# Kernel tuning notes

Measured on AMD Instinct MI355X. Metric: run time of the kernel, lower is better.

Reference implementation:

```python
import jax, jax.numpy as jnp
import numpy as np
import math

B, T, C = 8, 4096, 768
N_LAYER, LAYER_ID = 12, 6
LN_EPS = 1e-5


def wkv(w, u, k, v):
    """Numerically-stable RWKV-4 WKV recurrence.
    w, u: [C] (per-channel decay / bonus); k, v: [B, T, C] -> y: [B, T, C]."""
    kT = jnp.swapaxes(k, 0, 1)  # [T, B, C]
    vT = jnp.swapaxes(v, 0, 1)

    def step(carry, kv):
        aa, bb, pp = carry
        kt, vt = kv
        ww = u + kt
        p = jnp.maximum(pp, ww)
        e1 = jnp.exp(pp - p)
        e2 = jnp.exp(ww - p)
        y = (e1 * aa + e2 * vt) / (e1 * bb + e2)
        ww2 = w + pp
        p2 = jnp.maximum(ww2, kt)
        e1b = jnp.exp(ww2 - p2)
        e2b = jnp.exp(kt - p2)
        return (e1b * aa + e2b * vt, e1b * bb + e2b, p2), y

    zeros = jnp.zeros((k.shape[0], k.shape[2]), k.dtype)
    init = (zeros, zeros, jnp.full_like(zeros, -1e38))
    _, yT = jax.lax.scan(step, init, (kT, vT))
    return jnp.swapaxes(yT, 0, 1)  # [B, T, C]


def setup_inputs():
    key = jax.random.key(0)
    ks = jax.random.split(key, 8)
    # fancy init of spatial_decay / spatial_first (matches torch __init__)
    ratio = LAYER_ID / max(N_LAYER - 1, 1)
    h = np.arange(C, dtype=np.float64)
    decay = -5 + 8 * (h / max(C - 1, 1)) ** (0.7 + 1.3 * ratio)
    zigzag = np.array([(i + 1) % 3 - 1 for i in range(C)], dtype=np.float64) * 0.5
    first = np.ones(C) * math.log(0.3) + zigzag
    s = C ** -0.5
    return {
        "x_seq": jax.random.normal(ks[0], (B, T, C), jnp.float32),
        "scan_indices": jax.random.permutation(ks[1], T).astype(jnp.int32),
        "spatial_decay": jnp.asarray(decay, jnp.float32),
        "spatial_first": jnp.asarray(first, jnp.float32),
        "Wk": jax.random.normal(ks[2], (C, C), jnp.float32) * s,
        "Wv": jax.random.normal(ks[3], (C, C), jnp.float32) * s,
        "Wr": jax.random.normal(ks[4], (C, C), jnp.float32) * s,
        "Wo": jax.random.normal(ks[5], (C, C), jnp.float32) * s,
        "ln_g": jnp.ones((C,), jnp.float32),
        "ln_b": jnp.zeros((C,), jnp.float32),
    }


def reference(x_seq, scan_indices, spatial_decay, spatial_first, Wk, Wv, Wr, Wo, ln_g, ln_b):
    L = x_seq.shape[1]
    k = jnp.einsum('blc,dc->bld', x_seq, Wk)
    v = jnp.einsum('blc,dc->bld', x_seq, Wv)
    r = jnp.einsum('blc,dc->bld', x_seq, Wr)
    sr = jax.nn.sigmoid(r)
    # gather along sequence per scan order
    k_s = jnp.take(k, scan_indices, axis=1)
    v_s = jnp.take(v, scan_indices, axis=1)
    rwkv = wkv(spatial_decay / L, spatial_first / L, k_s, v_s)
    inv = jnp.argsort(scan_indices)
    rwkv = jnp.take(rwkv, inv, axis=1)
    # LayerNorm (key_norm)
    mu = jnp.mean(rwkv, axis=-1, keepdims=True)
    var = jnp.var(rwkv, axis=-1, keepdims=True)
    rwkv = (rwkv - mu) * jax.lax.rsqrt(var + LN_EPS) * ln_g + ln_b
    rwkv = sr * rwkv
    return jnp.einsum('blc,dc->bld', rwkv, Wo)
```

## Files before the change

kernel.cpp:

```cpp
#include <hip/hip_runtime.h>
#include <cstddef>
#include <cstdint>

#define B_DIM 8
#define T_SEQ 4096
#define C_DIM 768
#define M_ROWS (B_DIM * T_SEQ)
#define CC (C_DIM * C_DIM)
#define NCH 32
#define CHL (T_SEQ / NCH)

using bf16x8 = __attribute__((ext_vector_type(8))) short;
using f32x4  = __attribute__((ext_vector_type(4))) float;

static __device__ __forceinline__ unsigned short f2bf(float f) {
  unsigned int u = __float_as_uint(f);
  return (unsigned short)((u + 0x7fffu + ((u >> 16) & 1u)) >> 16);
}
static __device__ __forceinline__ float bf2f(unsigned short s) {
  return __uint_as_float(((unsigned int)s) << 16);
}

static __device__ __forceinline__ void gload_lds16(const void* g, void* l) {
  __builtin_amdgcn_global_load_lds(
      (const __attribute__((address_space(1))) unsigned int*)g,
      (__attribute__((address_space(3))) unsigned int*)l, 16, 0, 0);
}

__global__ __launch_bounds__(256) void convert_x(
    const float4* __restrict__ x, ushort4* __restrict__ xh)
{
  int i = blockIdx.x * 256 + threadIdx.x;
  float4 v = x[i];
  ushort4 h;
  h.x = f2bf(v.x); h.y = f2bf(v.y); h.z = f2bf(v.z); h.w = f2bf(v.w);
  xh[i] = h;
}

__global__ __launch_bounds__(256) void convert_w4(
    const float4* __restrict__ w0, const float4* __restrict__ w1,
    const float4* __restrict__ w2, const float4* __restrict__ w3,
    ushort4* __restrict__ dst)
{
  const int z = blockIdx.y;
  const float4* __restrict__ src = (z == 0) ? w0 : (z == 1) ? w1 : (z == 2) ? w2 : w3;
  int i = blockIdx.x * 256 + threadIdx.x;
  float4 v = src[i];
  ushort4 h;
  h.x = f2bf(v.x); h.y = f2bf(v.y); h.z = f2bf(v.z); h.w = f2bf(v.w);
  dst[(size_t)z * (CC / 4) + i] = h;
}

#define STG_A(DB, TAU, KH) do {                                            \
    const int ko_ = (TAU) * 64 + (KH) * 32;                                \
    short* d_ = lds + (((DB) + (KH) * 16384 + wave * 1024) >> 1);          \
    gload_lds16(pA_h0 + ko_, d_);                                          \
    gload_lds16(pA_h1 + ko_, d_ + 4096);                                   \
  } while (0)
#define STG_B(DB, TAU, KH) do {                                            \
    const int ko_ = (TAU) * 64 + (KH) * 32;                                \
    short* d_ = lds + (((DB) + 32768 + (KH) * 16384 + wave * 1024) >> 1);  \
    gload_lds16(pW_h0 + ko_, d_);                                          \
    gload_lds16(pW_h1 + ko_, d_ + 4096);                                   \
  } while (0)

#define MPHASE(DB, KHOFF, STAGE, CKPT)                                     \
  {                                                                        \
    _Pragma("unroll")                                                      \
    for (int mi = 0; mi < 8; ++mi)                                         \
      a[mi] = *(const bf16x8*)(lds +                                       \
          (((DB) + (KHOFF) + aoff + mi * 1024) >> 1));                     \
    _Pragma("unroll")                                                      \
    for (int ni = 0; ni < 4; ++ni)                                         \
      b[ni] = *(const bf16x8*)(lds +                                       \
          (((DB) + 32768 + (KHOFF) + boff + ni * 1024) >> 1));             \
    STAGE;                                                                 \
    __builtin_amdgcn_s_barrier();                                          \
    asm volatile("s_waitcnt lgkmcnt(0)" ::: "memory");                     \
    __builtin_amdgcn_sched_barrier(0);                                     \
    __builtin_amdgcn_s_setprio(1);                                         \
    _Pragma("unroll")                                                      \
    for (int mi = 0; mi < 8; ++mi)                                         \
      _Pragma("unroll")                                                    \
      for (int ni = 0; ni < 4; ++ni)                                       \
        acc[mi][ni] = __builtin_amdgcn_mfma_f32_16x16x32_bf16(             \
            a[mi], b[ni], acc[mi][ni], 0, 0, 0);                           \
    __builtin_amdgcn_s_setprio(0);                                         \
    CKPT;                                                                  \
    __builtin_amdgcn_s_barrier();                                          \
  }

template<int MODE>
__global__ __launch_bounds__(512, 2) void gemm8p(
    const short* __restrict__ A, const short* __restrict__ Wb,
    unsigned short* __restrict__ OK, unsigned short* __restrict__ OV,
    unsigned short* __restrict__ OSR, float* __restrict__ Oout)
{
  extern __shared__ short lds[];
  const int K = C_DIM;
  constexpr int NWN = (MODE == 0) ? 9 : 3;
  constexpr int CPX = (MODE == 0) ? 144 : 48;

  int f  = blockIdx.x + blockIdx.y * NWN;
  int wg = (f & 7) * CPX + (f >> 3);
  const int n0 = (wg % NWN) * 256;
  const int m0 = (wg / NWN) * 256;

  const int tid  = threadIdx.x;
  const int lane = tid & 63, wave = tid >> 6;
  const int wr = wave >> 2, wc = wave & 3;
  const int lr = lane & 15, lk = lane >> 4;

  const int aswz = lk ^ ((lr >> 1) & 3);
  const int aoff = wr * 8192 + lr * 64 + aswz * 16;
  const int boff = (wc >> 1) * 8192 + (wc & 1) * 4096 + lr * 64 + aswz * 16;

  const int srow = wave * 16 + (lane >> 2);
  const int skq  = (lane & 3) ^ ((lane >> 3) & 3);
  const short* pA_h0 = A + (size_t)(m0 + srow) * K + skq * 8;
  const short* pA_h1 = pA_h0 + (size_t)128 * K;
  const short* pW_h0 = Wb + (size_t)(n0 + srow) * K + skq * 8;
  const short* pW_h1 = pW_h0 + (size_t)128 * K;

  f32x4 acc[8][4];
#pragma unroll
  for (int i = 0; i < 8; ++i)
#pragma unroll
    for (int j = 0; j < 4; ++j) acc[i][j] = (f32x4){0.f, 0.f, 0.f, 0.f};

  STG_A(0, 0, 0); STG_B(0, 0, 0); STG_A(0, 0, 1); STG_B(0, 0, 1);
  STG_A(65536, 1, 0); STG_B(65536, 1, 0); STG_A(65536, 1, 1); STG_B(65536, 1, 1);
  asm volatile("s_waitcnt vmcnt(8)" ::: "memory");
  __builtin_amdgcn_s_barrier();

  bf16x8 a[8], b[4];
#pragma unroll
  for (int it = 0; it < 6; ++it) {
    MPHASE(0, 0,
        if (it >= 1) { STG_A(65536, 2 * it + 1, 1); STG_B(65536, 2 * it + 1, 1); }, )
    MPHASE(0, 16384,
        if (it < 5) { STG_A(0, 2 * it + 2, 0); STG_B(0, 2 * it + 2, 0); },
        if (it < 5) { asm volatile("s_waitcnt vmcnt(4)" ::: "memory"); }
        else        { asm volatile("s_waitcnt vmcnt(0)" ::: "memory"); })
    MPHASE(65536, 0,
        if (it < 5) { STG_A(0, 2 * it + 2, 1); STG_B(0, 2 * it + 2, 1); }, )
    MPHASE(65536, 16384,
        if (it < 5) { STG_A(65536, 2 * it + 3, 0); STG_B(65536, 2 * it + 3, 0); },
        if (it < 5) { asm volatile("s_waitcnt vmcnt(4)" ::: "memory"); })
  }

  if (MODE == 0) {
    const int which = n0 / 768;
    const int nc = (n0 % 768) + wc * 64;
    unsigned short* __restrict__ D = (which == 0) ? OK : (which == 1) ? OV : OSR;
#pragma unroll
    for (int mi = 0; mi < 8; ++mi)
#pragma unroll
      for (int ni = 0; ni < 4; ++ni) {
        const int row = m0 + wr * 128 + mi * 16 + lk * 4;
        const int col = nc + ni * 16 + lr;
#pragma unroll
        for (int j = 0; j < 4; ++j) {
          float v = acc[mi][ni][j];
          if (which == 2) v = 1.f / (1.f + __expf(-v));
          D[(size_t)(row + j) * C_DIM + col] = f2bf(v);
        }
      }
  } else {
#pragma unroll
    for (int mi = 0; mi < 8; ++mi)
#pragma unroll
      for (int ni = 0; ni < 4; ++ni) {
        const int row = m0 + wr * 128 + mi * 16 + lk * 4;
        const int col = n0 + wc * 64 + ni * 16 + lr;
#pragma unroll
        for (int j = 0; j < 4; ++j)
          Oout[(size_t)(row + j) * C_DIM + col] = acc[mi][ni][j];
      }
  }
}

#define P1_LOAD(kk_, vv_, base_)                                  \
  _Pragma("unroll") for (int j = 0; j < 8; ++j) {                 \
    int r_ = si[(base_) + j];                                     \
    kk_[j] = Kb[(size_t)r_ * C_DIM];                              \
    vv_[j] = Vb[(size_t)r_ * C_DIM];                              \
  }
#define P1_COMP(kk_, vv_)                                         \
  _Pragma("unroll") for (int j = 0; j < 8; ++j) {                 \
    float kt = bf2f(kk_[j]), vt = bf2f(vv_[j]);                   \
    float ww2 = w + pp; float p2 = fmaxf(ww2, kt);                \
    float e1b = __expf(ww2 - p2), e2b = __expf(kt - p2);          \
    aa = e1b * aa + e2b * vt; bb = e1b * bb + e2b; pp = p2;       \
  }

__global__ __launch_bounds__(256) void wkv_pass1(
    const unsigned short* __restrict__ Kin, const unsigned short* __restrict__ Vin,
    const int* __restrict__ sidx, const float* __restrict__ decay,
    float* __restrict__ aL, float* __restrict__ bL, float* __restrict__ pL)
{
  __shared__ int si[CHL];
  const int tid = threadIdx.x;
  const int ch = blockIdx.x, b = blockIdx.z;
  const int c = blockIdx.y * 256 + tid;
  if (tid < CHL) si[tid] = sidx[ch * CHL + tid];
  __syncthreads();
  const float w = decay[c] * (1.0f / (float)T_SEQ);
  const unsigned short* Kb = Kin + (size_t)b * T_SEQ * C_DIM + c;
  const unsigned short* Vb = Vin + (size_t)b * T_SEQ * C_DIM + c;
  float aa = 0.f, bb = 0.f, pp = -1e38f;
  unsigned short kA[8], vA[8], kB[8], vB[8];
  P1_LOAD(kA, vA, 0)
  for (int t0 = 0; t0 < CHL; t0 += 16) {
    P1_LOAD(kB, vB, t0 + 8)
    P1_COMP(kA, vA)
    if (t0 + 16 < CHL) { P1_LOAD(kA, vA, t0 + 16) }
    P1_COMP(kB, vB)
  }
  const int idx = (b * C_DIM + c) * NCH + ch;
  aL[idx] = aa; bL[idx] = bb; pL[idx] = pp;
}

__global__ __launch_bounds__(256) void wkv_scan(
    const float* __restrict__ aL, const float* __restrict__ bL,
    const float* __restrict__ pL,
    float* __restrict__ aI, float* __restrict__ bI, float* __restrict__ pI,
    const float* __restrict__ decay)
{
  const int g = blockIdx.x * 256 + threadIdx.x;
  const int c = g % C_DIM;
  const float wL = decay[c] * ((float)CHL / (float)T_SEQ);
  float aa = 0.f, bb = 0.f, pp = -1e38f;
  const int base = g * NCH;
  for (int ch = 0; ch < NCH; ++ch) {
    aI[base + ch] = aa; bI[base + ch] = bb; pI[base + ch] = pp;
    float p1 = pp + wL;
    float p2 = pL[base + ch];
    float p  = fmaxf(p1, p2);
    float e1 = __expf(p1 - p), e2 = __expf(p2 - p);
    aa = e1 * aa + e2 * aL[base + ch];
    bb = e1 * bb + e2 * bL[base + ch];
    pp = p;
  }
}

#define P2_LOAD(rr_, kk_, vv_, base_)                             \
  _Pragma("unroll") for (int j = 0; j < 8; ++j) {                 \
    int r_ = si[(base_) + j];                                     \
    rr_[j] = r_;                                                  \
    kk_[j] = Kb[(size_t)r_ * C_DIM];                              \
    vv_[j] = Vb[(size_t)r_ * C_DIM];                              \
  }
#define P2_COMP(rr_, kk_, vv_)                                    \
  _Pragma("unroll") for (int j = 0; j < 8; ++j) {                 \
    float kt = bf2f(kk_[j]), vt = bf2f(vv_[j]);                   \
    float ww = u + kt; float p = fmaxf(pp, ww);                   \
    float e1 = __expf(pp - p), e2 = __expf(ww - p);               \
    float y = (e1 * aa + e2 * vt) / (e1 * bb + e2);               \
    Yb[(size_t)rr_[j] * C_DIM] = f2bf(y);                         \
    float ww2 = w + pp; float p2 = fmaxf(ww2, kt);                \
    float e1b = __expf(ww2 - p2), e2b = __expf(kt - p2);          \
    aa = e1b * aa + e2b * vt; bb = e1b * bb + e2b; pp = p2;       \
  }

__global__ __launch_bounds__(256) void wkv_pass2(
    const unsigned short* __restrict__ Kin, const unsigned short* __restrict__ Vin,
    const int* __restrict__ sidx,
    const float* __restrict__ decay, const float* __restrict__ first,
    const float* __restrict__ aI, const float* __restrict__ bI,
    const float* __restrict__ pI, unsigned short* __restrict__ Y)
{
  __shared__ int si[CHL];
  const int tid = threadIdx.x;
  const int ch = blockIdx.x, b = blockIdx.z;
  const int c = blockIdx.y * 256 + tid;
  if (tid < CHL) si[tid] = sidx[ch * CHL + tid];
  __syncthreads();
  const float w = decay[c] * (1.0f / (float)T_SEQ);
  const float u = first[c] * (1.0f / (float)T_SEQ);
  const unsigned short* Kb = Kin + (size_t)b * T_SEQ * C_DIM + c;
  const unsigned short* Vb = Vin + (size_t)b * T_SEQ * C_DIM + c;
  unsigned short* Yb = Y + (size_t)b * T_SEQ * C_DIM + c;
  const int idx = (b * C_DIM + c) * NCH + ch;
  float aa = aI[idx], bb = bI[idx], pp = pI[idx];
  int rA[8], rB[8]; unsigned short kA[8], vA[8], kB[8], vB[8];
  P2_LOAD(rA, kA, vA, 0)
  for (int t0 = 0; t0 < CHL; t0 += 16) {
    P2_LOAD(rB, kB, vB, t0 + 8)
    P2_COMP(rA, kA, vA)
    if (t0 + 16 < CHL) { P2_LOAD(rA, kA, vA, t0 + 16) }
    P2_COMP(rB, kB, vB)
  }
}

__global__ __launch_bounds__(256) void ln_gate(
    const unsigned short* __restrict__ Y, const unsigned short* __restrict__ SR,
    const float* __restrict__ gam, const float* __restrict__ bet,
    unsigned short* __restrict__ G)
{
  const size_t row = blockIdx.x;
  const unsigned short* x = Y + row * C_DIM;
  const unsigned short* sr = SR + row * C_DIM;
  unsigned short* go = G + row * C_DIM;
  const int tid = threadIdx.x;

  float vals[3];
  float s = 0.f, s2 = 0.f;
#pragma unroll
  for (int j = 0; j < 3; ++j) {
    float v = bf2f(x[tid + j * 256]);
    vals[j] = v;
    s += v; s2 += v * v;
  }
#pragma unroll
  for (int off = 32; off >= 1; off >>= 1) {
    s  += __shfl_xor(s, off, 64);
    s2 += __shfl_xor(s2, off, 64);
  }
  __shared__ float red[8];
  const int wid = tid >> 6;
  if ((tid & 63) == 0) { red[wid] = s; red[wid + 4] = s2; }
  __syncthreads();
  s  = red[0] + red[1] + red[2] + red[3];
  s2 = red[4] + red[5] + red[6] + red[7];

  const float mu   = s * (1.f / (float)C_DIM);
  const float var  = s2 * (1.f / (float)C_DIM) - mu * mu;
  const float rsig = rsqrtf(var + 1e-5f);

#pragma unroll
  for (int j = 0; j < 3; ++j) {
    const int cc = tid + j * 256;
    float yv = (vals[j] - mu) * rsig * gam[cc] + bet[cc];
    go[cc] = f2bf(yv * bf2f(sr[cc]));
  }
}

extern "C" void kernel_launch(void* const* d_in, const int* in_sizes, int n_in,
                              void* d_out, int out_size, void* d_ws, size_t ws_size,
                              hipStream_t stream) {
  const float* x     = (const float*)d_in[0];
  const int*   sidx  = (const int*)  d_in[1];
  const float* decay = (const float*)d_in[2];
  const float* first = (const float*)d_in[3];
  const float* Wk    = (const float*)d_in[4];
  const float* Wv    = (const float*)d_in[5];
  const float* Wr    = (const float*)d_in[6];
  const float* Wo    = (const float*)d_in[7];
  const float* ln_g  = (const float*)d_in[8];
  const float* ln_b  = (const float*)d_in[9];
  float* out = (float*)d_out;

  const size_t NE = (size_t)M_ROWS * C_DIM;
  short* Whs  = (short*)d_ws;
  short* x_hi = Whs + 4 * (size_t)CC;
  unsigned short* Ybuf = (unsigned short*)x_hi;
  unsigned short* Kbuf = (unsigned short*)(x_hi + NE);
  unsigned short* Gbuf = Kbuf;
  unsigned short* Vbuf = Kbuf + NE;
  unsigned short* SRb  = Vbuf + NE;
  float* aL = (float*)(SRb + NE);
  float* bL = aL + 196608;
  float* pL = bL + 196608;
  float* aI = pL + 196608;
  float* bI = aI + 196608;
  float* pI = bI + 196608;

  (void)hipFuncSetAttribute(reinterpret_cast<const void*>(&gemm8p<0>),
                            hipFuncAttributeMaxDynamicSharedMemorySize, 131072);
  (void)hipFuncSetAttribute(reinterpret_cast<const void*>(&gemm8p<1>),
                            hipFuncAttributeMaxDynamicSharedMemorySize, 131072);

  convert_x<<<24576, 256, 0, stream>>>((const float4*)x, (ushort4*)x_hi);
  convert_w4<<<dim3(576, 4), 256, 0, stream>>>(
      (const float4*)Wk, (const float4*)Wv, (const float4*)Wr, (const float4*)Wo,
      (ushort4*)Whs);

  gemm8p<0><<<dim3(9, 128), 512, 131072, stream>>>(
      x_hi, Whs, Kbuf, Vbuf, SRb, nullptr);

  wkv_pass1<<<dim3(NCH, 3, B_DIM), 256, 0, stream>>>(Kbuf, Vbuf, sidx, decay, aL, bL, pL);
  wkv_scan<<<24, 256, 0, stream>>>(aL, bL, pL, aI, bI, pI, decay);
  wkv_pass2<<<dim3(NCH, 3, B_DIM), 256, 0, stream>>>(Kbuf, Vbuf, sidx, decay, first,
                                                     aI, bI, pI, Ybuf);
  ln_gate<<<M_ROWS, 256, 0, stream>>>(Ybuf, SRb, ln_g, ln_b, Gbuf);
  gemm8p<1><<<dim3(3, 128), 512, 131072, stream>>>(
      (const short*)Gbuf, Whs + 3 * (size_t)CC, nullptr, nullptr, nullptr, out);
}
```

Baseline: 319.6 us.

## Fuse LayerNorm and gating into WKV pass2; register-prefetch LDS fragments in GEMM

The WKV second pass now runs one 768-thread block per (chunk, batch), so each block holds a full row of channels. It computes LayerNorm and the sigmoid gate inline at each timestep using wave shuffles plus a block-level reduction, and writes the gated output directly, which removes the separate ln_gate kernel and its Y buffer round trip. The cost is a __syncthreads per timestep inside the serial recurrence. Separately, the GEMM main loop is restructured with double-buffered register fragments: the next K-slice is read from LDS while MFMAs run on the current one, with three stages of global-to-LDS prefetch and one barrier per phase instead of two.

```diff
diff --git a/kernel.cpp b/kernel.cpp
--- a/kernel.cpp
+++ b/kernel.cpp
@@ -63,35 +63,31 @@
     gload_lds16(pW_h0 + ko_, d_);                                          \
     gload_lds16(pW_h1 + ko_, d_ + 4096);                                   \
   } while (0)
-
-#define MPHASE(DB, KHOFF, STAGE, CKPT)                                     \
-  {                                                                        \
+#define STG_R(R) do {                                                      \
+    STG_A((((R) >> 1) & 1) * 65536, (R) >> 1, (R) & 1);                    \
+    STG_B((((R) >> 1) & 1) * 65536, (R) >> 1, (R) & 1);                    \
+  } while (0)
+
+#define READF(AA, BB, R) do {                                              \
+    const int db_ = (((R) >> 1) & 1) * 65536 + ((R) & 1) * 16384;          \
     _Pragma("unroll")                                                      \
     for (int mi = 0; mi < 8; ++mi)                                         \
-      a[mi] = *(const bf16x8*)(lds +                                       \
-          (((DB) + (KHOFF) + aoff + mi * 1024) >> 1));                     \
+      AA[mi] = *(const bf16x8*)(lds + ((db_ + aoff + mi * 1024) >> 1));    \
     _Pragma("unroll")                                                      \
     for (int ni = 0; ni < 4; ++ni)                                         \
-      b[ni] = *(const bf16x8*)(lds +                                       \
-          (((DB) + 32768 + (KHOFF) + boff + ni * 1024) >> 1));             \
-    STAGE;                                                                 \
-    __builtin_amdgcn_s_barrier();                                          \
-    asm volatile("s_waitcnt lgkmcnt(0)" ::: "memory");                     \
-    __builtin_amdgcn_sched_barrier(0);                                     \
-    __builtin_amdgcn_s_setprio(1);                                         \
+      BB[ni] = *(const bf16x8*)(lds + ((db_ + 32768 + boff + ni * 1024) >> 1)); \
+  } while (0)
+
+#define MM(AA, BB)                                                         \
     _Pragma("unroll")                                                      \
     for (int mi = 0; mi < 8; ++mi)                                         \
       _Pragma("unroll")                                                    \
       for (int ni = 0; ni < 4; ++ni)                                       \
         acc[mi][ni] = __builtin_amdgcn_mfma_f32_16x16x32_bf16(             \
-            a[mi], b[ni], acc[mi][ni], 0, 0, 0);                           \
-    __builtin_amdgcn_s_setprio(0);                                         \
-    CKPT;                                                                  \
-    __builtin_amdgcn_s_barrier();                                          \
-  }
+            AA[mi], BB[ni], acc[mi][ni], 0, 0, 0);
 
 template<int MODE>
-__global__ __launch_bounds__(512, 2) void gemm8p(
+__global__ __launch_bounds__(512, 2) void gemmPF(
     const short* __restrict__ A, const short* __restrict__ Wb,
     unsigned short* __restrict__ OK, unsigned short* __restrict__ OV,
     unsigned short* __restrict__ OSR, float* __restrict__ Oout)
@@ -128,25 +124,29 @@
 #pragma unroll
     for (int j = 0; j < 4; ++j) acc[i][j] = (f32x4){0.f, 0.f, 0.f, 0.f};
 
-  STG_A(0, 0, 0); STG_B(0, 0, 0); STG_A(0, 0, 1); STG_B(0, 0, 1);
-  STG_A(65536, 1, 0); STG_B(65536, 1, 0); STG_A(65536, 1, 1); STG_B(65536, 1, 1);
-  asm volatile("s_waitcnt vmcnt(8)" ::: "memory");
+  bf16x8 aX[8], bX[4], aY[8], bY[4];
+
+  STG_R(0); STG_R(1); STG_R(2);
+  asm volatile("s_waitcnt vmcnt(4)" ::: "memory");
   __builtin_amdgcn_s_barrier();
-
-  bf16x8 a[8], b[4];
-#pragma unroll
-  for (int it = 0; it < 6; ++it) {
-    MPHASE(0, 0,
-        if (it >= 1) { STG_A(65536, 2 * it + 1, 1); STG_B(65536, 2 * it + 1, 1); }, )
-    MPHASE(0, 16384,
-        if (it < 5) { STG_A(0, 2 * it + 2, 0); STG_B(0, 2 * it + 2, 0); },
-        if (it < 5) { asm volatile("s_waitcnt vmcnt(4)" ::: "memory"); }
-        else        { asm volatile("s_waitcnt vmcnt(0)" ::: "memory"); })
-    MPHASE(65536, 0,
-        if (it < 5) { STG_A(0, 2 * it + 2, 1); STG_B(0, 2 * it + 2, 1); }, )
-    MPHASE(65536, 16384,
-        if (it < 5) { STG_A(65536, 2 * it + 3, 0); STG_B(65536, 2 * it + 3, 0); },
-        if (it < 5) { asm volatile("s_waitcnt vmcnt(4)" ::: "memory"); })
+  __builtin_amdgcn_sched_barrier(0);
+  READF(aX, bX, 0);
+  __builtin_amdgcn_sched_barrier(0);
+
+#pragma unroll
+  for (int p = 0; p < 24; ++p) {
+    if (p < 23) {
+      if (p & 1) { READF(aX, bX, p + 1); } else { READF(aY, bY, p + 1); }
+    }
+    if (p <= 20) STG_R(p + 3);
+    __builtin_amdgcn_sched_barrier(0);
+    __builtin_amdgcn_s_setprio(1);
+    if (p & 1) { MM(aY, bY) } else { MM(aX, bX) }
+    __builtin_amdgcn_s_setprio(0);
+    if (p <= 20)      { asm volatile("s_waitcnt vmcnt(4)" ::: "memory"); }
+    else if (p == 21) { asm volatile("s_waitcnt vmcnt(0)" ::: "memory"); }
+    __builtin_amdgcn_s_barrier();
+    __builtin_amdgcn_sched_barrier(0);
   }
 
   if (MODE == 0) {
@@ -244,95 +244,81 @@
   }
 }
 
-#define P2_LOAD(rr_, kk_, vv_, base_)                             \
+#define P2F_LOAD(rr_, kk_, vv_, ss_, base_)                       \
   _Pragma("unroll") for (int j = 0; j < 8; ++j) {                 \
     int r_ = si[(base_) + j];                                     \
     rr_[j] = r_;                                                  \
     kk_[j] = Kb[(size_t)r_ * C_DIM];                              \
     vv_[j] = Vb[(size_t)r_ * C_DIM];                              \
-  }
-#define P2_COMP(rr_, kk_, vv_)                                    \
+    ss_[j] = Sb[(size_t)r_ * C_DIM];                              \
+  }
+
+#define P2F_COMP(rr_, kk_, vv_, ss_)                              \
   _Pragma("unroll") for (int j = 0; j < 8; ++j) {                 \
     float kt = bf2f(kk_[j]), vt = bf2f(vv_[j]);                   \
     float ww = u + kt; float p = fmaxf(pp, ww);                   \
     float e1 = __expf(pp - p), e2 = __expf(ww - p);               \
-    float y = (e1 * aa + e2 * vt) / (e1 * bb + e2);               \
-    Yb[(size_t)rr_[j] * C_DIM] = f2bf(y);                         \
+    float y = (e1 * aa + e2 * vt) / (e1 * bbs + e2);              \
+    float s1 = y, s2v = y * y;                                    \
+    _Pragma("unroll")                                             \
+    for (int off = 32; off >= 1; off >>= 1) {                     \
+      s1  += __shfl_xor(s1, off, 64);                             \
+      s2v += __shfl_xor(s2v, off, 64);                            \
+    }                                                             \
+    if (lane == 0) { red[j & 1][0][wid] = s1; red[j & 1][1][wid] = s2v; } \
+    __syncthreads();                                              \
+    float ts = 0.f, ts2 = 0.f;                                    \
+    _Pragma("unroll")                                             \
+    for (int wv = 0; wv < 12; ++wv) {                             \
+      ts  += red[j & 1][0][wv];                                   \
+      ts2 += red[j & 1][1][wv];                                   \
+    }                                                             \
+    const float mu  = ts * (1.f / (float)C_DIM);                  \
+    const float var = ts2 * (1.f / (float)C_DIM) - mu * mu;       \
+    const float rs  = rsqrtf(var + 1e-5f);                        \
+    const float yln = (y - mu) * rs * gg + bb0;                   \
+    Gb[(size_t)rr_[j] * C_DIM] = f2bf(yln * bf2f(ss_[j]));        \
     float ww2 = w + pp; float p2 = fmaxf(ww2, kt);                \
     float e1b = __expf(ww2 - p2), e2b = __expf(kt - p2);          \
-    aa = e1b * aa + e2b * vt; bb = e1b * bb + e2b; pp = p2;       \
-  }
-
-__global__ __launch_bounds__(256) void wkv_pass2(
+    aa = e1b * aa + e2b * vt; bbs = e1b * bbs + e2b; pp = p2;     \
+  }
+
+__global__ __launch_bounds__(768) void wkv_pass2_ln(
     const unsigned short* __restrict__ Kin, const unsigned short* __restrict__ Vin,
     const int* __restrict__ sidx,
     const float* __restrict__ decay, const float* __restrict__ first,
     const float* __restrict__ aI, const float* __restrict__ bI,
-    const float* __restrict__ pI, unsigned short* __restrict__ Y)
+    const float* __restrict__ pI,
+    const unsigned short* __restrict__ SR,
+    const float* __restrict__ gam, const float* __restrict__ bet,
+    unsigned short* __restrict__ G)
 {
   __shared__ int si[CHL];
+  __shared__ float red[2][2][12];
   const int tid = threadIdx.x;
-  const int ch = blockIdx.x, b = blockIdx.z;
-  const int c = blockIdx.y * 256 + tid;
+  const int ch = blockIdx.x, b = blockIdx.y;
   if (tid < CHL) si[tid] = sidx[ch * CHL + tid];
   __syncthreads();
+  const int c = tid;
+  const int lane = tid & 63, wid = tid >> 6;
   const float w = decay[c] * (1.0f / (float)T_SEQ);
   const float u = first[c] * (1.0f / (float)T_SEQ);
+  const float gg = gam[c], bb0 = bet[c];
   const unsigned short* Kb = Kin + (size_t)b * T_SEQ * C_DIM + c;
   const unsigned short* Vb = Vin + (size_t)b * T_SEQ * C_DIM + c;
-  unsigned short* Yb = Y + (size_t)b * T_SEQ * C_DIM + c;
+  const unsigned short* Sb = SR + (size_t)b * T_SEQ * C_DIM + c;
+  unsigned short* Gb = G + (size_t)b * T_SEQ * C_DIM + c;
   const int idx = (b * C_DIM + c) * NCH + ch;
-  float aa = aI[idx], bb = bI[idx], pp = pI[idx];
-  int rA[8], rB[8]; unsigned short kA[8], vA[8], kB[8], vB[8];
-  P2_LOAD(rA, kA, vA, 0)
+  float aa = aI[idx], bbs = bI[idx], pp = pI[idx];
+
+  int rA[8], rB[8];
+  unsigned short kA[8], vA[8], sA[8], kB[8], vB[8], sB[8];
+  P2F_LOAD(rA, kA, vA, sA, 0)
   for (int t0 = 0; t0 < CHL; t0 += 16) {
-    P2_LOAD(rB, kB, vB, t0 + 8)
-    P2_COMP(rA, kA, vA)
-    if (t0 + 16 < CHL) { P2_LOAD(rA, kA, vA, t0 + 16) }
-    P2_COMP(rB, kB, vB)
-  }
-}
-
-__global__ __launch_bounds__(256) void ln_gate(
-    const unsigned short* __restrict__ Y, const unsigned short* __restrict__ SR,
-    const float* __restrict__ gam, const float* __restrict__ bet,
-    unsigned short* __restrict__ G)
-{
-  const size_t row = blockIdx.x;
-  const unsigned short* x = Y + row * C_DIM;
-  const unsigned short* sr = SR + row * C_DIM;
-  unsigned short* go = G + row * C_DIM;
-  const int tid = threadIdx.x;
-
-  float vals[3];
-  float s = 0.f, s2 = 0.f;
-#pragma unroll
-  for (int j = 0; j < 3; ++j) {
-    float v = bf2f(x[tid + j * 256]);
-    vals[j] = v;
-    s += v; s2 += v * v;
-  }
-#pragma unroll
-  for (int off = 32; off >= 1; off >>= 1) {
-    s  += __shfl_xor(s, off, 64);
-    s2 += __shfl_xor(s2, off, 64);
-  }
-  __shared__ float red[8];
-  const int wid = tid >> 6;
-  if ((tid & 63) == 0) { red[wid] = s; red[wid + 4] = s2; }
-  __syncthreads();
-  s  = red[0] + red[1] + red[2] + red[3];
-  s2 = red[4] + red[5] + red[6] + red[7];
-
-  const float mu   = s * (1.f / (float)C_DIM);
-  const float var  = s2 * (1.f / (float)C_DIM) - mu * mu;
-  const float rsig = rsqrtf(var + 1e-5f);
-
-#pragma unroll
-  for (int j = 0; j < 3; ++j) {
-    const int cc = tid + j * 256;
-    float yv = (vals[j] - mu) * rsig * gam[cc] + bet[cc];
-    go[cc] = f2bf(yv * bf2f(sr[cc]));
+    P2F_LOAD(rB, kB, vB, sB, t0 + 8)
+    P2F_COMP(rA, kA, vA, sA)
+    if (t0 + 16 < CHL) { P2F_LOAD(rA, kA, vA, sA, t0 + 16) }
+    P2F_COMP(rB, kB, vB, sB)
   }
 }
 
@@ -354,21 +340,20 @@
   const size_t NE = (size_t)M_ROWS * C_DIM;
   short* Whs  = (short*)d_ws;
   short* x_hi = Whs + 4 * (size_t)CC;
-  unsigned short* Ybuf = (unsigned short*)x_hi;
   unsigned short* Kbuf = (unsigned short*)(x_hi + NE);
-  unsigned short* Gbuf = Kbuf;
   unsigned short* Vbuf = Kbuf + NE;
   unsigned short* SRb  = Vbuf + NE;
-  float* aL = (float*)(SRb + NE);
+  unsigned short* Gbuf = SRb + NE;
+  float* aL = (float*)(Gbuf + NE);
   float* bL = aL + 196608;
   float* pL = bL + 196608;
   float* aI = pL + 196608;
   float* bI = aI + 196608;
   float* pI = bI + 196608;
 
-  (void)hipFuncSetAttribute(reinterpret_cast<const void*>(&gemm8p<0>),
+  (void)hipFuncSetAttribute(reinterpret_cast<const void*>(&gemmPF<0>),
                             hipFuncAttributeMaxDynamicSharedMemorySize, 131072);
-  (void)hipFuncSetAttribute(reinterpret_cast<const void*>(&gemm8p<1>),
+  (void)hipFuncSetAttribute(reinterpret_cast<const void*>(&gemmPF<1>),
                             hipFuncAttributeMaxDynamicSharedMemorySize, 131072);
 
   convert_x<<<24576, 256, 0, stream>>>((const float4*)x, (ushort4*)x_hi);
@@ -376,14 +361,14 @@
       (const float4*)Wk, (const float4*)Wv, (const float4*)Wr, (const float4*)Wo,
       (ushort4*)Whs);
 
-  gemm8p<0><<<dim3(9, 128), 512, 131072, stream>>>(
+  gemmPF<0><<<dim3(9, 128), 512, 131072, stream>>>(
       x_hi, Whs, Kbuf, Vbuf, SRb, nullptr);
 
   wkv_pass1<<<dim3(NCH, 3, B_DIM), 256, 0, stream>>>(Kbuf, Vbuf, sidx, decay, aL, bL, pL);
   wkv_scan<<<24, 256, 0, stream>>>(aL, bL, pL, aI, bI, pI, decay);
-  wkv_pass2<<<dim3(NCH, 3, B_DIM), 256, 0, stream>>>(Kbuf, Vbuf, sidx, decay, first,
-                                                     aI, bI, pI, Ybuf);
-  ln_gate<<<M_ROWS, 256, 0, stream>>>(Ybuf, SRb, ln_g, ln_b, Gbuf);
-  gemm8p<1><<<dim3(3, 128), 512, 131072, stream>>>(
+  wkv_pass2_ln<<<dim3(NCH, B_DIM), 768, 0, stream>>>(
+      Kbuf, Vbuf, sidx, decay, first, aI, bI, pI, SRb, ln_g, ln_b, Gbuf);
+
+  gemmPF<1><<<dim3(3, 128), 512, 131072, stream>>>(
       (const short*)Gbuf, Whs + 3 * (size_t)CC, nullptr, nullptr, nullptr, out);
 }
```

Result: slower. 380.2 us (+18.9%).

## Double-buffer LDS fragment reads in registers and deepen the global prefetch

Applied to the files above, without the earlier changes.

Restructures the GEMM main loop into 24 half-tile phases. The LDS-to-register fragment reads for the next phase go into a second register set (aX/bX vs aY/bY), so they overlap the current MFMA block instead of waiting on lgkmcnt before the math. Global-to-LDS staging now runs three half-stages ahead, and there is one barrier per phase instead of two. The extra fragment registers raise register pressure at 2 blocks per CU, and the tighter buffer reuse distance could race if the wait counts are off.

```diff
diff --git a/kernel.cpp b/kernel.cpp
--- a/kernel.cpp
+++ b/kernel.cpp
@@ -63,35 +63,31 @@
     gload_lds16(pW_h0 + ko_, d_);                                          \
     gload_lds16(pW_h1 + ko_, d_ + 4096);                                   \
   } while (0)
-
-#define MPHASE(DB, KHOFF, STAGE, CKPT)                                     \
-  {                                                                        \
+#define STG_R(R) do {                                                      \
+    STG_A((((R) >> 1) & 1) * 65536, (R) >> 1, (R) & 1);                    \
+    STG_B((((R) >> 1) & 1) * 65536, (R) >> 1, (R) & 1);                    \
+  } while (0)
+
+#define READF(AA, BB, R) do {                                              \
+    const int db_ = (((R) >> 1) & 1) * 65536 + ((R) & 1) * 16384;          \
     _Pragma("unroll")                                                      \
     for (int mi = 0; mi < 8; ++mi)                                         \
-      a[mi] = *(const bf16x8*)(lds +                                       \
-          (((DB) + (KHOFF) + aoff + mi * 1024) >> 1));                     \
+      AA[mi] = *(const bf16x8*)(lds + ((db_ + aoff + mi * 1024) >> 1));    \
     _Pragma("unroll")                                                      \
     for (int ni = 0; ni < 4; ++ni)                                         \
-      b[ni] = *(const bf16x8*)(lds +                                       \
-          (((DB) + 32768 + (KHOFF) + boff + ni * 1024) >> 1));             \
-    STAGE;                                                                 \
-    __builtin_amdgcn_s_barrier();                                          \
-    asm volatile("s_waitcnt lgkmcnt(0)" ::: "memory");                     \
-    __builtin_amdgcn_sched_barrier(0);                                     \
-    __builtin_amdgcn_s_setprio(1);                                         \
+      BB[ni] = *(const bf16x8*)(lds + ((db_ + 32768 + boff + ni * 1024) >> 1)); \
+  } while (0)
+
+#define MM(AA, BB)                                                         \
     _Pragma("unroll")                                                      \
     for (int mi = 0; mi < 8; ++mi)                                         \
       _Pragma("unroll")                                                    \
       for (int ni = 0; ni < 4; ++ni)                                       \
         acc[mi][ni] = __builtin_amdgcn_mfma_f32_16x16x32_bf16(             \
-            a[mi], b[ni], acc[mi][ni], 0, 0, 0);                           \
-    __builtin_amdgcn_s_setprio(0);                                         \
-    CKPT;                                                                  \
-    __builtin_amdgcn_s_barrier();                                          \
-  }
+            AA[mi], BB[ni], acc[mi][ni], 0, 0, 0);
 
 template<int MODE>
-__global__ __launch_bounds__(512, 2) void gemm8p(
+__global__ __launch_bounds__(512, 2) void gemmPF(
     const short* __restrict__ A, const short* __restrict__ Wb,
     unsigned short* __restrict__ OK, unsigned short* __restrict__ OV,
     unsigned short* __restrict__ OSR, float* __restrict__ Oout)
@@ -128,25 +124,29 @@
 #pragma unroll
     for (int j = 0; j < 4; ++j) acc[i][j] = (f32x4){0.f, 0.f, 0.f, 0.f};
 
-  STG_A(0, 0, 0); STG_B(0, 0, 0); STG_A(0, 0, 1); STG_B(0, 0, 1);
-  STG_A(65536, 1, 0); STG_B(65536, 1, 0); STG_A(65536, 1, 1); STG_B(65536, 1, 1);
-  asm volatile("s_waitcnt vmcnt(8)" ::: "memory");
+  bf16x8 aX[8], bX[4], aY[8], bY[4];
+
+  STG_R(0); STG_R(1); STG_R(2);
+  asm volatile("s_waitcnt vmcnt(4)" ::: "memory");
   __builtin_amdgcn_s_barrier();
-
-  bf16x8 a[8], b[4];
-#pragma unroll
-  for (int it = 0; it < 6; ++it) {
-    MPHASE(0, 0,
-        if (it >= 1) { STG_A(65536, 2 * it + 1, 1); STG_B(65536, 2 * it + 1, 1); }, )
-    MPHASE(0, 16384,
-        if (it < 5) { STG_A(0, 2 * it + 2, 0); STG_B(0, 2 * it + 2, 0); },
-        if (it < 5) { asm volatile("s_waitcnt vmcnt(4)" ::: "memory"); }
-        else        { asm volatile("s_waitcnt vmcnt(0)" ::: "memory"); })
-    MPHASE(65536, 0,
-        if (it < 5) { STG_A(0, 2 * it + 2, 1); STG_B(0, 2 * it + 2, 1); }, )
-    MPHASE(65536, 16384,
-        if (it < 5) { STG_A(65536, 2 * it + 3, 0); STG_B(65536, 2 * it + 3, 0); },
-        if (it < 5) { asm volatile("s_waitcnt vmcnt(4)" ::: "memory"); })
+  __builtin_amdgcn_sched_barrier(0);
+  READF(aX, bX, 0);
+  __builtin_amdgcn_sched_barrier(0);
+
+#pragma unroll
+  for (int p = 0; p < 24; ++p) {
+    if (p < 23) {
+      if (p & 1) { READF(aX, bX, p + 1); } else { READF(aY, bY, p + 1); }
+    }
+    if (p <= 20) STG_R(p + 3);
+    __builtin_amdgcn_sched_barrier(0);
+    __builtin_amdgcn_s_setprio(1);
+    if (p & 1) { MM(aY, bY) } else { MM(aX, bX) }
+    __builtin_amdgcn_s_setprio(0);
+    if (p <= 20)      { asm volatile("s_waitcnt vmcnt(4)" ::: "memory"); }
+    else if (p == 21) { asm volatile("s_waitcnt vmcnt(0)" ::: "memory"); }
+    __builtin_amdgcn_s_barrier();
+    __builtin_amdgcn_sched_barrier(0);
   }
 
   if (MODE == 0) {
@@ -366,9 +366,9 @@
   float* bI = aI + 196608;
   float* pI = bI + 196608;
 
-  (void)hipFuncSetAttribute(reinterpret_cast<const void*>(&gemm8p<0>),
+  (void)hipFuncSetAttribute(reinterpret_cast<const void*>(&gemmPF<0>),
                             hipFuncAttributeMaxDynamicSharedMemorySize, 131072);
-  (void)hipFuncSetAttribute(reinterpret_cast<const void*>(&gemm8p<1>),
+  (void)hipFuncSetAttribute(reinterpret_cast<const void*>(&gemmPF<1>),
                             hipFuncAttributeMaxDynamicSharedMemorySize, 131072);
 
   convert_x<<<24576, 256, 0, stream>>>((const float4*)x, (ushort4*)x_hi);
@@ -376,7 +376,7 @@
       (const float4*)Wk, (const float4*)Wv, (const float4*)Wr, (const float4*)Wo,
       (ushort4*)Whs);
 
-  gemm8p<0><<<dim3(9, 128), 512, 131072, stream>>>(
+  gemmPF<0><<<dim3(9, 128), 512, 131072, stream>>>(
       x_hi, Whs, Kbuf, Vbuf, SRb, nullptr);
 
   wkv_pass1<<<dim3(NCH, 3, B_DIM), 256, 0, stream>>>(Kbuf, Vbuf, sidx, decay, aL, bL, pL);
@@ -384,6 +384,6 @@
   wkv_pass2<<<dim3(NCH, 3, B_DIM), 256, 0, stream>>>(Kbuf, Vbuf, sidx, decay, first,
                                                      aI, bI, pI, Ybuf);
   ln_gate<<<M_ROWS, 256, 0, stream>>>(Ybuf, SRb, ln_g, ln_b, Gbuf);
-  gemm8p<1><<<dim3(3, 128), 512, 131072, stream>>>(
+  gemmPF<1><<<dim3(3, 128), 512, 131072, stream>>>(
       (const short*)Gbuf, Whs + 3 * (size_t)CC, nullptr, nullptr, nullptr, out);
 }
```

Result: no change. 313.4 us (-2.0%).

## Restructure GEMM to 256x128 tiles with 3-stage K-pipeline and 4 waves

Applied to the files above, without the earlier changes.

Replaces the 512-thread 256x256-tile GEMM, which double-buffers 64-wide K slices, with a 256-thread 256x128-tile kernel. The new kernel uses a three-buffer ring of 32-wide K slices, prefetching two slices ahead with one barrier per phase. LDS per block drops from 128KB to 72KB and the grid doubles, aiming for better occupancy and latency hiding. The cost is more blocks reloading A tiles and smaller per-block reuse of the weight tile. The epilogue index math still has to line up with the new wave layout.

```diff
diff --git a/kernel.cpp b/kernel.cpp
--- a/kernel.cpp
+++ b/kernel.cpp
@@ -51,76 +51,80 @@
   dst[(size_t)z * (CC / 4) + i] = h;
 }
 
-#define STG_A(DB, TAU, KH) do {                                            \
-    const int ko_ = (TAU) * 64 + (KH) * 32;                                \
-    short* d_ = lds + (((DB) + (KH) * 16384 + wave * 1024) >> 1);          \
-    gload_lds16(pA_h0 + ko_, d_);                                          \
-    gload_lds16(pA_h1 + ko_, d_ + 4096);                                   \
-  } while (0)
-#define STG_B(DB, TAU, KH) do {                                            \
-    const int ko_ = (TAU) * 64 + (KH) * 32;                                \
-    short* d_ = lds + (((DB) + 32768 + (KH) * 16384 + wave * 1024) >> 1);  \
-    gload_lds16(pW_h0 + ko_, d_);                                          \
-    gload_lds16(pW_h1 + ko_, d_ + 4096);                                   \
-  } while (0)
-
-#define MPHASE(DB, KHOFF, STAGE, CKPT)                                     \
-  {                                                                        \
+#define STG3(R) do { if ((R) < 24) {                                       \
+    const int rbs_ = ((R) % 3) * 12288;                        \
+    const int ko_ = (R) * 32;                                              \
+    short* da_ = lds + rbs_ + wave * 512;                                  \
+    gload_lds16(pAs + ko_, da_);                                           \
+    gload_lds16(pAs +  64 * 768 + ko_, da_ + 2048);                        \
+    gload_lds16(pAs + 128 * 768 + ko_, da_ + 4096);                        \
+    gload_lds16(pAs + 192 * 768 + ko_, da_ + 6144);                        \
+    short* db_ = lds + rbs_ + 8192 + wave * 512;                           \
+    gload_lds16(pBs + ko_, db_);                                           \
+    gload_lds16(pBs +  64 * 768 + ko_, db_ + 2048);                        \
+  } } while (0)
+
+#define RDF(R) do {                                                        \
+    const int rb_ = ((R) % 3) * 24576;                          \
     _Pragma("unroll")                                                      \
     for (int mi = 0; mi < 8; ++mi)                                         \
-      a[mi] = *(const bf16x8*)(lds +                                       \
-          (((DB) + (KHOFF) + aoff + mi * 1024) >> 1));                     \
+      a[mi] = *(const bf16x8*)(lds + ((rb_ + abase + mi * 1024) >> 1));    \
     _Pragma("unroll")                                                      \
     for (int ni = 0; ni < 4; ++ni)                                         \
-      b[ni] = *(const bf16x8*)(lds +                                       \
-          (((DB) + 32768 + (KHOFF) + boff + ni * 1024) >> 1));             \
-    STAGE;                                                                 \
-    __builtin_amdgcn_s_barrier();                                          \
-    asm volatile("s_waitcnt lgkmcnt(0)" ::: "memory");                     \
-    __builtin_amdgcn_sched_barrier(0);                                     \
-    __builtin_amdgcn_s_setprio(1);                                         \
+      b[ni] = *(const bf16x8*)(lds + ((rb_ + bbase + ni * 1024) >> 1));    \
+  } while (0)
+
+#define MM()                                                               \
     _Pragma("unroll")                                                      \
     for (int mi = 0; mi < 8; ++mi)                                         \
       _Pragma("unroll")                                                    \
       for (int ni = 0; ni < 4; ++ni)                                       \
         acc[mi][ni] = __builtin_amdgcn_mfma_f32_16x16x32_bf16(             \
-            a[mi], b[ni], acc[mi][ni], 0, 0, 0);                           \
+            a[mi], b[ni], acc[mi][ni], 0, 0, 0);
+
+#define PH3(P)                                                             \
+  {                                                                        \
+    RDF(P);                                                                \
+    STG3((P) + 2);                                                         \
+    __builtin_amdgcn_sched_barrier(0);                                     \
+    __builtin_amdgcn_s_setprio(1);                                         \
+    MM()                                                                   \
     __builtin_amdgcn_s_setprio(0);                                         \
-    CKPT;                                                                  \
+    if ((P) <= 21)      { asm volatile("s_waitcnt vmcnt(6)" ::: "memory"); } \
+    else if ((P) == 22) { asm volatile("s_waitcnt vmcnt(0)" ::: "memory"); } \
     __builtin_amdgcn_s_barrier();                                          \
+    __builtin_amdgcn_sched_barrier(0);                                     \
   }
 
 template<int MODE>
-__global__ __launch_bounds__(512, 2) void gemm8p(
+__global__ __launch_bounds__(256, 2) void gemmDB(
     const short* __restrict__ A, const short* __restrict__ Wb,
     unsigned short* __restrict__ OK, unsigned short* __restrict__ OV,
     unsigned short* __restrict__ OSR, float* __restrict__ Oout)
 {
   extern __shared__ short lds[];
   const int K = C_DIM;
-  constexpr int NWN = (MODE == 0) ? 9 : 3;
-  constexpr int CPX = (MODE == 0) ? 144 : 48;
+  constexpr int NWN = (MODE == 0) ? 18 : 6;
+  constexpr int CPX = (MODE == 0) ? 288 : 96;
 
   int f  = blockIdx.x + blockIdx.y * NWN;
   int wg = (f & 7) * CPX + (f >> 3);
-  const int n0 = (wg % NWN) * 256;
+  const int n0 = (wg % NWN) * 128;
   const int m0 = (wg / NWN) * 256;
 
   const int tid  = threadIdx.x;
   const int lane = tid & 63, wave = tid >> 6;
-  const int wr = wave >> 2, wc = wave & 3;
+  const int wr = wave >> 1, wc = wave & 1;
   const int lr = lane & 15, lk = lane >> 4;
 
   const int aswz = lk ^ ((lr >> 1) & 3);
-  const int aoff = wr * 8192 + lr * 64 + aswz * 16;
-  const int boff = (wc >> 1) * 8192 + (wc & 1) * 4096 + lr * 64 + aswz * 16;
-
-  const int srow = wave * 16 + (lane >> 2);
-  const int skq  = (lane & 3) ^ ((lane >> 3) & 3);
-  const short* pA_h0 = A + (size_t)(m0 + srow) * K + skq * 8;
-  const short* pA_h1 = pA_h0 + (size_t)128 * K;
-  const short* pW_h0 = Wb + (size_t)(n0 + srow) * K + skq * 8;
-  const short* pW_h1 = pW_h0 + (size_t)128 * K;
+  const int abase = (wr * 128 + lr) * 64 + aswz * 16;
+  const int bbase = 16384 + (wc * 64 + lr) * 64 + aswz * 16;
+
+  const int srow = tid >> 2;
+  const int skq  = (tid & 3) ^ ((tid >> 3) & 3);
+  const short* pAs = A  + (size_t)(m0 + srow) * K + skq * 8;
+  const short* pBs = Wb + (size_t)(n0 + srow) * K + skq * 8;
 
   f32x4 acc[8][4];
 #pragma unroll
@@ -128,26 +132,15 @@
 #pragma unroll
     for (int j = 0; j < 4; ++j) acc[i][j] = (f32x4){0.f, 0.f, 0.f, 0.f};
 
-  STG_A(0, 0, 0); STG_B(0, 0, 0); STG_A(0, 0, 1); STG_B(0, 0, 1);
-  STG_A(65536, 1, 0); STG_B(65536, 1, 0); STG_A(65536, 1, 1); STG_B(65536, 1, 1);
-  asm volatile("s_waitcnt vmcnt(8)" ::: "memory");
+  bf16x8 a[8], b[4];
+
+  STG3(0); STG3(1);
+  asm volatile("s_waitcnt vmcnt(6)" ::: "memory");
   __builtin_amdgcn_s_barrier();
-
-  bf16x8 a[8], b[4];
-#pragma unroll
-  for (int it = 0; it < 6; ++it) {
-    MPHASE(0, 0,
-        if (it >= 1) { STG_A(65536, 2 * it + 1, 1); STG_B(65536, 2 * it + 1, 1); }, )
-    MPHASE(0, 16384,
-        if (it < 5) { STG_A(0, 2 * it + 2, 0); STG_B(0, 2 * it + 2, 0); },
-        if (it < 5) { asm volatile("s_waitcnt vmcnt(4)" ::: "memory"); }
-        else        { asm volatile("s_waitcnt vmcnt(0)" ::: "memory"); })
-    MPHASE(65536, 0,
-        if (it < 5) { STG_A(0, 2 * it + 2, 1); STG_B(0, 2 * it + 2, 1); }, )
-    MPHASE(65536, 16384,
-        if (it < 5) { STG_A(65536, 2 * it + 3, 0); STG_B(65536, 2 * it + 3, 0); },
-        if (it < 5) { asm volatile("s_waitcnt vmcnt(4)" ::: "memory"); })
-  }
+  __builtin_amdgcn_sched_barrier(0);
+
+#pragma unroll
+  for (int p = 0; p < 24; ++p) PH3(p)
 
   if (MODE == 0) {
     const int which = n0 / 768;
@@ -366,17 +359,17 @@
   float* bI = aI + 196608;
   float* pI = bI + 196608;
 
-  (void)hipFuncSetAttribute(reinterpret_cast<const void*>(&gemm8p<0>),
-                            hipFuncAttributeMaxDynamicSharedMemorySize, 131072);
-  (void)hipFuncSetAttribute(reinterpret_cast<const void*>(&gemm8p<1>),
-                            hipFuncAttributeMaxDynamicSharedMemorySize, 131072);
+  (void)hipFuncSetAttribute(reinterpret_cast<const void*>(&gemmDB<0>),
+                            hipFuncAttributeMaxDynamicSharedMemorySize, 73728);
+  (void)hipFuncSetAttribute(reinterpret_cast<const void*>(&gemmDB<1>),
+                            hipFuncAttributeMaxDynamicSharedMemorySize, 73728);
 
   convert_x<<<24576, 256, 0, stream>>>((const float4*)x, (ushort4*)x_hi);
   convert_w4<<<dim3(576, 4), 256, 0, stream>>>(
       (const float4*)Wk, (const float4*)Wv, (const float4*)Wr, (const float4*)Wo,
       (ushort4*)Whs);
 
-  gemm8p<0><<<dim3(9, 128), 512, 131072, stream>>>(
+  gemmDB<0><<<dim3(18, 128), 256, 73728, stream>>>(
       x_hi, Whs, Kbuf, Vbuf, SRb, nullptr);
 
   wkv_pass1<<<dim3(NCH, 3, B_DIM), 256, 0, stream>>>(Kbuf, Vbuf, sidx, decay, aL, bL, pL);
@@ -384,6 +377,6 @@
   wkv_pass2<<<dim3(NCH, 3, B_DIM), 256, 0, stream>>>(Kbuf, Vbuf, sidx, decay, first,
                                                      aI, bI, pI, Ybuf);
   ln_gate<<<M_ROWS, 256, 0, stream>>>(Ybuf, SRb, ln_g, ln_b, Gbuf);
-  gemm8p<1><<<dim3(3, 128), 512, 131072, stream>>>(
+  gemmDB<1><<<dim3(6, 128), 256, 73728, stream>>>(
       (const short*)Gbuf, Whs + 3 * (size_t)CC, nullptr, nullptr, nullptr, out);
 }
```

After: 310.0 us (median of 2 runs). 1.03x faster.
